# Optimization experiments

Hardware: AMD Instinct MI355X
Metric: run time of the kernel (lower is better)

Reference implementation:

```python
import jax, jax.numpy as jnp
import numpy as np

VOCAB = 50000
EDIM = 128
CDIM = 128
B = 512
LEVEL_FACTORS = [4, 4, 3, 3, 2, 1]  # 7 levels total, N = 403968 nodes


def _build_forest():
    """Deterministic random forest: per-level arrays of token, global parent idx, depth, batch id."""
    rng = np.random.default_rng(0)
    level_sizes = [B]
    for f in LEVEL_FACTORS:
        level_sizes.append(level_sizes[-1] * f)
    offsets = np.cumsum([0] + level_sizes)
    tokens = [rng.integers(0, VOCAB, B)]
    parent = [np.zeros(B, np.int64)]          # roots: dummy parent (depth 0 never scattered)
    depth = [np.zeros(B, np.int64)]
    batch_id = [np.arange(B)]
    for d in range(1, len(level_sizes)):
        n = level_sizes[d]
        tokens.append(rng.integers(0, VOCAB, n))
        p_local = rng.integers(0, level_sizes[d - 1], n)
        parent.append(offsets[d - 1] + p_local)
        depth.append(np.full(n, d, np.int64))
        batch_id.append(batch_id[d - 1][p_local])
    cat = lambda xs: np.concatenate(xs).astype(np.int32)
    return cat(tokens), cat(parent), cat(depth), cat(batch_id), len(level_sizes)


def setup_inputs() -> dict:
    key = jax.random.key(0)
    k1, k2, k3 = jax.random.split(key, 3)
    emb_table = jax.random.normal(k1, (VOCAB, EDIM), dtype=jnp.float32) * 0.02
    W = jax.random.normal(k2, (CDIM, EDIM), dtype=jnp.float32) * 0.02
    b = jax.random.normal(k3, (CDIM,), dtype=jnp.float32) * 0.02
    tokens, parent, depth, batch_id, num_levels = _build_forest()
    return {
        "emb_table": emb_table,
        "W": W,
        "b": b,
        "tokens": jnp.asarray(tokens),
        "parent": jnp.asarray(parent),
        "depth": jnp.asarray(depth),
        "batch_id": jnp.asarray(batch_id),
        "num_levels": num_levels,
        "batch_size": B,
    }


def reference(emb_table, W, b, tokens, parent, depth, batch_id, num_levels, batch_size):
    N = tokens.shape[0]
    # per-node base: W_c(embedding(token))  [N, CDIM]
    base = emb_table[tokens] @ W.T + b
    h = base
    # bottom-up subtree sum, level-batched scatter-add (deepest level first)
    for d in range(num_levels - 1, 0, -1):
        contrib = jnp.where((depth == d)[:, None], h, 0.0)
        h = h + jax.ops.segment_sum(contrib, parent, num_segments=N)
    # per-batch elementwise max over all nodes of the tree, clamped at 0
    # (original maxes zero-initialized snapshots over all recursion calls)
    out = jax.ops.segment_max(h, batch_id, num_segments=batch_size)
    return jnp.maximum(out, 0.0)
```

## Files before the change

### kernel.cpp

```cpp
#include <hip/hip_runtime.h>
#include <hip/hip_bf16.h>


using f32x4   = __attribute__((ext_vector_type(4))) float;
using short8  = __attribute__((ext_vector_type(8))) short;
using ushort8 = __attribute__((ext_vector_type(8))) unsigned short;
using float4v = __attribute__((ext_vector_type(4))) float;

#define N_ALL   403968
#define N_NONRT 403456
#define N_PAR   256512
#define OFF3    10752
#define OFF4    35328
#define OFF5    109056
#define OFF6    256512
#define SEG5    108544
#define LEAFSEG 256000
#define NVOCAB  50000
#define CAPW    384
#define D1CAP   24
#define D2CAP   64
#define WEMB_BLOCKS 782

__device__ __forceinline__ short f2bf(float f) {
  union { float f; unsigned u; } v; v.f = f;
  unsigned r = v.u + 0x7fffu + ((v.u >> 16) & 1u);
  return (short)(r >> 16);
}
__device__ __forceinline__ float bf2f(unsigned short u) {
  union { unsigned u; float f; } v; v.u = ((unsigned)u) << 16; return v.f;
}

__global__ __launch_bounds__(256) void prep_k(const float* __restrict__ W,
                                              const float* __restrict__ emb,
                                              const float* __restrict__ bias,
                                              unsigned short* __restrict__ Wemb,
                                              const int* __restrict__ parent,
                                              int* __restrict__ cnt) {
  if (blockIdx.x >= WEMB_BLOCKS) {
    int i = (blockIdx.x - WEMB_BLOCKS) * 256 + threadIdx.x + 512;
    atomicAdd(cnt + parent[i], 1);
    return;
  }
  __shared__ short WBs[16384];
  for (int idx = threadIdx.x; idx < 16384; idx += 256) {
    int j = idx & 7, c16 = (idx >> 3) & 15, g = (idx >> 7) & 3,
        s = (idx >> 9) & 3, t = idx >> 11;
    WBs[idx] = f2bf(W[(t * 16 + c16) * 128 + s * 32 + g * 8 + j]);
  }
  __syncthreads();

  const int tid = threadIdx.x, lane = tid & 63, wv = tid >> 6;
  const int l15 = lane & 15, g = lane >> 4;
  const int nb = blockIdx.x * 64 + wv * 16;

  f32x4 acc[8];
  #pragma unroll
  for (int t = 0; t < 8; ++t) {
    const float bb = bias[t * 16 + l15];
    #pragma unroll
    for (int j = 0; j < 4; ++j) acc[t][j] = bb;
  }
  int vr = nb + l15; if (vr > NVOCAB - 1) vr = NVOCAB - 1;
  const float* erow = emb + (size_t)vr * 128;
  short8 a[4];
  #pragma unroll
  for (int s = 0; s < 4; ++s) {
    float4v f0 = *(const float4v*)(erow + s * 32 + g * 8);
    float4v f1 = *(const float4v*)(erow + s * 32 + g * 8 + 4);
    short8 t;
    t[0] = f2bf(f0[0]); t[1] = f2bf(f0[1]); t[2] = f2bf(f0[2]); t[3] = f2bf(f0[3]);
    t[4] = f2bf(f1[0]); t[5] = f2bf(f1[1]); t[6] = f2bf(f1[2]); t[7] = f2bf(f1[3]);
    a[s] = t;
  }
  #pragma unroll
  for (int t = 0; t < 8; ++t) {
    #pragma unroll
    for (int s = 0; s < 4; ++s) {
      const short8 bfr = *(const short8*)&WBs[((((t * 4 + s) * 4) + g) * 16 + l15) * 8];
      acc[t] = __builtin_amdgcn_mfma_f32_16x16x32_bf16(a[s], bfr, acc[t], 0, 0, 0);
    }
  }
  #pragma unroll
  for (int j = 0; j < 4; ++j) {
    const int r = nb + g * 4 + j;
    if (r < NVOCAB) {
      ushort8 hv;
      #pragma unroll
      for (int t = 0; t < 8; ++t) hv[t] = (unsigned short)f2bf(acc[t][j]);
      *(ushort8*)(Wemb + (size_t)r * 128 + l15 * 8) = hv;
    }
  }
}

__device__ __forceinline__ int block_excl_scan(int v, int* total) {
  int lane = threadIdx.x & 63, wv = threadIdx.x >> 6;
  int x = v;
  #pragma unroll
  for (int d = 1; d < 64; d <<= 1) { int y = __shfl_up(x, d); if (lane >= d) x += y; }
  __shared__ int ws[4];
  if (lane == 63) ws[wv] = x;
  __syncthreads();
  int off = 0;
  for (int w = 0; w < wv; ++w) off += ws[w];
  __syncthreads();
  if (total) { int t = 0; for (int w = 0; w < 4; ++w) t += ws[w]; *total = t; }
  return x + off - v;
}

__global__ __launch_bounds__(256) void scanA(const int* __restrict__ cnt,
                                             int* __restrict__ start,
                                             int* __restrict__ bsum) {
  int i = blockIdx.x * 256 + threadIdx.x;
  int v = cnt[i];
  int tot;
  int ex = block_excl_scan(v, &tot);
  start[i] = ex;
  if (threadIdx.x == 0) bsum[blockIdx.x] = tot;
}

__global__ __launch_bounds__(256) void addcopy(int* __restrict__ start,
                                               int* __restrict__ start_mut,
                                               const int* __restrict__ bsum) {
  __shared__ int wsum[4];
  __shared__ int pfx;
  int partial = 0;
  for (int j = threadIdx.x; j < blockIdx.x; j += 256) partial += bsum[j];
  #pragma unroll
  for (int d = 32; d > 0; d >>= 1) partial += __shfl_down(partial, d);
  const int lane = threadIdx.x & 63, wv = threadIdx.x >> 6;
  if (lane == 0) wsum[wv] = partial;
  __syncthreads();
  if (threadIdx.x == 0) pfx = wsum[0] + wsum[1] + wsum[2] + wsum[3];
  __syncthreads();
  int i = blockIdx.x * 256 + threadIdx.x;
  int s = start[i] + pfx;
  start[i] = s; start_mut[i] = s;
  if (i == 0) start[N_PAR] = N_NONRT;
}

__global__ __launch_bounds__(256) void fill_k(const int* __restrict__ parent,
                                              const int* __restrict__ tokens,
                                              const int* __restrict__ start,
                                              int* __restrict__ start_mut,
                                              int* __restrict__ chlist,
                                              int* __restrict__ tok5s,
                                              int* __restrict__ meta5) {
  int i = blockIdx.x * 256 + threadIdx.x + 512;
  int p = atomicAdd(start_mut + parent[i], 1);
  chlist[p] = (i >= OFF6) ? tokens[i] : i;
  if (i >= OFF5 && i < OFF6) {
    const int s = p - SEG5;
    tok5s[s] = tokens[i];
    meta5[s] = ((start[i] - LEAFSEG) << 6) | (start[i + 1] - start[i]);
  }
}

__global__ __launch_bounds__(256, 8) void d4f_k(
    const unsigned short* __restrict__ Wemb,
    const int*   __restrict__ tokens,
    const int*   __restrict__ start,
    const int*   __restrict__ chlist,
    const int*   __restrict__ tok5s,
    const int*   __restrict__ meta5,
    unsigned short* __restrict__ Hout)
{
  const int chunk = threadIdx.x & 15;
  const int node  = threadIdx.x >> 4;
  const int nd    = blockIdx.x * 16 + node;
  const int gid   = OFF4 + nd;

  float acc[8], mx[8];
  {
    const int tok = tokens[gid];
    const ushort8 b = *(const ushort8*)(Wemb + (size_t)tok * 128 + chunk * 8);
    #pragma unroll
    for (int t = 0; t < 8; ++t) { acc[t] = bf2f(b[t]); mx[t] = 0.0f; }
  }

  const int s5 = start[gid] - SEG5;
  const int e5 = start[gid + 1] - SEG5;
  for (int c = s5; c < e5; ++c) {
    const int tok5 = tok5s[c];
    const int m    = meta5[c];
    const int lb   = LEAFSEG + (m >> 6);
    const int lc   = m & 63;
    const ushort8 r5 = *(const ushort8*)(Wemb + (size_t)tok5 * 128 + chunk * 8);
    float h5[8], lmx[8];
    #pragma unroll
    for (int t = 0; t < 8; ++t) { h5[t] = bf2f(r5[t]); lmx[t] = 0.0f; }
    for (int l = lb; l < lb + lc; ++l) {
      const int tl = chlist[l];
      const ushort8 rl = *(const ushort8*)(Wemb + (size_t)tl * 128 + chunk * 8);
      #pragma unroll
      for (int t = 0; t < 8; ++t) {
        const float hv = bf2f(rl[t]);
        h5[t] += hv;
        lmx[t] = fmaxf(lmx[t], hv);
      }
    }
    #pragma unroll
    for (int t = 0; t < 8; ++t) {
      acc[t] += h5[t];
      mx[t] = fmaxf(mx[t], fmaxf(lmx[t], h5[t]));
    }
  }

  ushort8 hv, mv;
  #pragma unroll
  for (int t = 0; t < 8; ++t) {
    hv[t] = (unsigned short)f2bf(acc[t]);
    mv[t] = (unsigned short)f2bf(fmaxf(mx[t], acc[t]));
  }
  __builtin_nontemporal_store(hv, (ushort8*)(Hout + (size_t)nd * 256 + chunk * 8));
  __builtin_nontemporal_store(mv, (ushort8*)(Hout + (size_t)nd * 256 + 128 + chunk * 8));
}

__global__ __launch_bounds__(256, 4) void d3_k(
    const unsigned short* __restrict__ Wemb,
    const int*   __restrict__ tokens,
    const unsigned short* __restrict__ Hin,
    unsigned short*       __restrict__ Hout,
    const int*   __restrict__ start,
    const int*   __restrict__ chlist)
{
  __shared__ int chl[CAPW];
  const int chunk = threadIdx.x & 15;
  const int node  = threadIdx.x >> 4;
  const int nd    = blockIdx.x * 16 + node;
  const int gid   = OFF3 + nd;

  int bcs = start[OFF3 + blockIdx.x * 16];
  const int bce = start[OFF3 + blockIdx.x * 16 + 16];
  const int nw  = bce - bcs;
  bool useLds = (nw <= CAPW);
  if (useLds)
    for (int i = threadIdx.x; i < nw; i += 256)
      chl[i] = chlist[bcs + i] - OFF4;
  __syncthreads();

  float acc[8], mx[8];
  {
    const int tok = tokens[gid];
    const ushort8 b = *(const ushort8*)(Wemb + (size_t)tok * 128 + chunk * 8);
    #pragma unroll
    for (int t = 0; t < 8; ++t) { acc[t] = bf2f(b[t]); mx[t] = 0.0f; }
  }

  int k = start[gid];
  const int e = start[gid + 1];
  for (; k + 2 <= e; k += 2) {
    int c0, c1;
    if (useLds) { c0 = chl[k - bcs]; c1 = chl[k + 1 - bcs]; }
    else        { c0 = chlist[k] - OFF4; c1 = chlist[k + 1] - OFF4; }
    const ushort8 h0 = *(const ushort8*)(Hin + (size_t)c0 * 256 + chunk * 8);
    const ushort8 m0 = *(const ushort8*)(Hin + (size_t)c0 * 256 + 128 + chunk * 8);
    const ushort8 h1 = *(const ushort8*)(Hin + (size_t)c1 * 256 + chunk * 8);
    const ushort8 m1 = *(const ushort8*)(Hin + (size_t)c1 * 256 + 128 + chunk * 8);
    #pragma unroll
    for (int t = 0; t < 8; ++t) {
      acc[t] += bf2f(h0[t]); mx[t] = fmaxf(mx[t], bf2f(m0[t]));
      acc[t] += bf2f(h1[t]); mx[t] = fmaxf(mx[t], bf2f(m1[t]));
    }
  }
  if (k < e) {
    int c0 = useLds ? chl[k - bcs] : chlist[k] - OFF4;
    const ushort8 h0 = *(const ushort8*)(Hin + (size_t)c0 * 256 + chunk * 8);
    const ushort8 m0 = *(const ushort8*)(Hin + (size_t)c0 * 256 + 128 + chunk * 8);
    #pragma unroll
    for (int t = 0; t < 8; ++t) {
      acc[t] += bf2f(h0[t]); mx[t] = fmaxf(mx[t], bf2f(m0[t]));
    }
  }

  ushort8 hv, mv;
  #pragma unroll
  for (int t = 0; t < 8; ++t) {
    hv[t] = (unsigned short)f2bf(acc[t]);
    mv[t] = (unsigned short)f2bf(fmaxf(mx[t], acc[t]));
  }
  *(ushort8*)(Hout + (size_t)nd * 256 + chunk * 8) = hv;
  *(ushort8*)(Hout + (size_t)nd * 256 + 128 + chunk * 8) = mv;
}

__global__ __launch_bounds__(256, 2) void top_k(
    const unsigned short* __restrict__ Wemb,
    const int*   __restrict__ tokens,
    const unsigned short* __restrict__ Hd3,
    float*       __restrict__ outf,
    const int*   __restrict__ start,
    const int*   __restrict__ chlist)
{
  __shared__ int d1id[D1CAP];
  __shared__ int c2[D1CAP];
  __shared__ int d2off[D1CAP + 1];
  __shared__ int d2id[D2CAP];
  __shared__ int n2s;
  __shared__ unsigned short rec2[D2CAP][256];
  __shared__ unsigned short rec1[D1CAP][256];

  const int r   = blockIdx.x;
  const int tid = threadIdx.x;
  const int chunk = tid & 15, grp = tid >> 4;

  const int s1 = start[r];
  int n1 = start[r + 1] - s1; if (n1 > D1CAP) n1 = D1CAP;
  if (tid < n1) {
    const int g1 = chlist[s1 + tid];
    d1id[tid] = g1;
    c2[tid] = start[g1 + 1] - start[g1];
  }
  __syncthreads();
  if (tid == 0) {
    int run = 0;
    for (int i = 0; i < n1; ++i) {
      d2off[i] = run; run += c2[i];
      if (run > D2CAP) run = D2CAP;
    }
    d2off[n1] = run; n2s = run;
  }
  __syncthreads();
  const int n2 = n2s;
  if (tid < n1) {
    const int g1 = d1id[tid];
    const int s = start[g1], o = d2off[tid], cmax = d2off[tid + 1] - o;
    for (int q = 0; q < cmax; ++q) d2id[o + q] = chlist[s + q];
  }
  __syncthreads();

  for (int i = grp; i < n2; i += 16) {
    const int g2 = d2id[i];
    float acc[8], mx[8];
    {
      const ushort8 b = *(const ushort8*)(Wemb + (size_t)tokens[g2] * 128 + chunk * 8);
      #pragma unroll
      for (int t = 0; t < 8; ++t) { acc[t] = bf2f(b[t]); mx[t] = 0.0f; }
    }
    const int e = start[g2 + 1];
    for (int k = start[g2]; k < e; ++k) {
      const int c3 = chlist[k] - OFF3;
      const ushort8 h0 = *(const ushort8*)(Hd3 + (size_t)c3 * 256 + chunk * 8);
      const ushort8 m0 = *(const ushort8*)(Hd3 + (size_t)c3 * 256 + 128 + chunk * 8);
      #pragma unroll
      for (int t = 0; t < 8; ++t) {
        acc[t] += bf2f(h0[t]); mx[t] = fmaxf(mx[t], bf2f(m0[t]));
      }
    }
    #pragma unroll
    for (int t = 0; t < 8; ++t) {
      rec2[i][chunk * 8 + t] = (unsigned short)f2bf(acc[t]);
      rec2[i][128 + chunk * 8 + t] =
          (unsigned short)f2bf(fmaxf(mx[t], acc[t]));
    }
  }
  __syncthreads();

  for (int i = grp; i < n1; i += 16) {
    const int g1 = d1id[i];
    float acc[8], mx[8];
    {
      const ushort8 b = *(const ushort8*)(Wemb + (size_t)tokens[g1] * 128 + chunk * 8);
      #pragma unroll
      for (int t = 0; t < 8; ++t) { acc[t] = bf2f(b[t]); mx[t] = 0.0f; }
    }
    for (int q = d2off[i]; q < d2off[i + 1]; ++q) {
      #pragma unroll
      for (int t = 0; t < 8; ++t) {
        acc[t] += bf2f(rec2[q][chunk * 8 + t]);
        mx[t] = fmaxf(mx[t], bf2f(rec2[q][128 + chunk * 8 + t]));
      }
    }
    #pragma unroll
    for (int t = 0; t < 8; ++t) {
      rec1[i][chunk * 8 + t] = (unsigned short)f2bf(acc[t]);
      rec1[i][128 + chunk * 8 + t] =
          (unsigned short)f2bf(fmaxf(mx[t], acc[t]));
    }
  }
  __syncthreads();

  if (grp == 0) {
    float acc[8], mx[8];
    {
      const ushort8 b = *(const ushort8*)(Wemb + (size_t)tokens[r] * 128 + chunk * 8);
      #pragma unroll
      for (int t = 0; t < 8; ++t) { acc[t] = bf2f(b[t]); mx[t] = 0.0f; }
    }
    for (int i = 0; i < n1; ++i) {
      #pragma unroll
      for (int t = 0; t < 8; ++t) {
        acc[t] += bf2f(rec1[i][chunk * 8 + t]);
        mx[t] = fmaxf(mx[t], bf2f(rec1[i][128 + chunk * 8 + t]));
      }
    }
    #pragma unroll
    for (int t = 0; t < 8; ++t)
      outf[(size_t)r * 128 + t * 16 + chunk] = fmaxf(mx[t], acc[t]);
  }
}

extern "C" void kernel_launch(void* const* d_in, const int* in_sizes, int n_in,
                              void* d_out, int out_size, void* d_ws, size_t ws_size,
                              hipStream_t stream) {
  (void)in_sizes; (void)n_in; (void)out_size; (void)ws_size;

  const float* emb    = (const float*)d_in[0];
  const float* W      = (const float*)d_in[1];
  const float* bias   = (const float*)d_in[2];
  const int*   tokens = (const int*)d_in[3];
  const int*   parent = (const int*)d_in[4];

  char* p = (char*)d_ws;
  unsigned short* bufB  = (unsigned short*)p;
  unsigned short* bufA  = (unsigned short*)(p + 75497472);
  int*   chlist   = (int*)(p + 113246208);
  int*   start    = (int*)(p + 114860032);
  int*   cnt      = (int*)(p + 115886084);
  int*   bsum     = (int*)(p + 116912132);
  unsigned short* Wemb = (unsigned short*)(p + 116949008);
  int*   tok5s    = (int*)(p + 129749008);
  int*   meta5    = (int*)(p + 130338832);

  float* outf = (float*)d_out;

  hipMemsetAsync(cnt, 0, (size_t)N_PAR * 4, stream);
  prep_k<<<WEMB_BLOCKS + N_NONRT / 256, 256, 0, stream>>>(
      W, emb, bias, Wemb, parent, cnt);
  scanA<<<N_PAR / 256, 256, 0, stream>>>(cnt, start, bsum);
  addcopy<<<N_PAR / 256, 256, 0, stream>>>(start, cnt , bsum);
  fill_k<<<N_NONRT / 256, 256, 0, stream>>>(parent, tokens, start,
                                            cnt , chlist,
                                            tok5s, meta5);

  d4f_k<<<73728 / 16, 256, 0, stream>>>(Wemb, tokens, start, chlist,
                                        tok5s, meta5, bufA);
  d3_k<<<24576 / 16, 256, 0, stream>>>(Wemb, tokens, bufA, bufB, start, chlist);
  top_k<<<512, 256, 0, stream>>>(Wemb, tokens, bufB, outf, start, chlist);
}
```

Measured before the change: 135.8 us.

## Map one wavefront per node in d4f and d3 kernels with scalar indices

Both the d4f and d3 kernels switch from 16 threads per node with 16-byte loads to one 64-lane wavefront per node, where each lane handles a 4-byte pair of bf16 values. The node index is made wave-uniform via readfirstlane, so child-list and metadata loads become scalar. The LDS staging of child indices in d3 is removed. This is meant to shorten the serial per-node loops and reduce divergence between nodes with different child counts, at the cost of narrower per-lane memory transactions and four times as many blocks.

```diff
diff --git a/kernel.cpp b/kernel.cpp
--- a/kernel.cpp
+++ b/kernel.cpp
@@ -17,7 +17,6 @@
 #define SEG5    108544
 #define LEAFSEG 256000
 #define NVOCAB  50000
-#define CAPW    384
 #define D1CAP   24
 #define D2CAP   64
 #define WEMB_BLOCKS 782
@@ -29,6 +28,12 @@
 }
 __device__ __forceinline__ float bf2f(unsigned short u) {
   union { unsigned u; float f; } v; v.u = ((unsigned)u) << 16; return v.f;
+}
+__device__ __forceinline__ float lo_bf(unsigned v) {
+  union { unsigned u; float f; } x; x.u = v << 16; return x.f;
+}
+__device__ __forceinline__ float hi_bf(unsigned v) {
+  union { unsigned u; float f; } x; x.u = v & 0xffff0000u; return x.f;
 }
 
 __global__ __launch_bounds__(256) void prep_k(const float* __restrict__ W,
@@ -165,17 +170,17 @@
     const int*   __restrict__ meta5,
     unsigned short* __restrict__ Hout)
 {
-  const int chunk = threadIdx.x & 15;
-  const int node  = threadIdx.x >> 4;
-  const int nd    = blockIdx.x * 16 + node;
-  const int gid   = OFF4 + nd;
-
-  float acc[8], mx[8];
+  const int lane = threadIdx.x & 63;
+  const int nd = __builtin_amdgcn_readfirstlane(blockIdx.x * 4 + (threadIdx.x >> 6));
+  const int gid = OFF4 + nd;
+
+  const unsigned* __restrict__ WembU = (const unsigned*)Wemb;
+
+  float acc0, acc1, mx0 = 0.0f, mx1 = 0.0f;
   {
     const int tok = tokens[gid];
-    const ushort8 b = *(const ushort8*)(Wemb + (size_t)tok * 128 + chunk * 8);
-    #pragma unroll
-    for (int t = 0; t < 8; ++t) { acc[t] = bf2f(b[t]); mx[t] = 0.0f; }
+    const unsigned bv = WembU[(size_t)tok * 64 + lane];
+    acc0 = lo_bf(bv); acc1 = hi_bf(bv);
   }
 
   const int s5 = start[gid] - SEG5;
@@ -185,38 +190,31 @@
     const int m    = meta5[c];
     const int lb   = LEAFSEG + (m >> 6);
     const int lc   = m & 63;
-    const ushort8 r5 = *(const ushort8*)(Wemb + (size_t)tok5 * 128 + chunk * 8);
-    float h5[8], lmx[8];
-    #pragma unroll
-    for (int t = 0; t < 8; ++t) { h5[t] = bf2f(r5[t]); lmx[t] = 0.0f; }
+    const unsigned r5 = WembU[(size_t)tok5 * 64 + lane];
+    float h0 = lo_bf(r5), h1 = hi_bf(r5);
+    float l0 = 0.0f, l1 = 0.0f;
     for (int l = lb; l < lb + lc; ++l) {
       const int tl = chlist[l];
-      const ushort8 rl = *(const ushort8*)(Wemb + (size_t)tl * 128 + chunk * 8);
-      #pragma unroll
-      for (int t = 0; t < 8; ++t) {
-        const float hv = bf2f(rl[t]);
-        h5[t] += hv;
-        lmx[t] = fmaxf(lmx[t], hv);
-      }
-    }
-    #pragma unroll
-    for (int t = 0; t < 8; ++t) {
-      acc[t] += h5[t];
-      mx[t] = fmaxf(mx[t], fmaxf(lmx[t], h5[t]));
-    }
-  }
-
-  ushort8 hv, mv;
-  #pragma unroll
-  for (int t = 0; t < 8; ++t) {
-    hv[t] = (unsigned short)f2bf(acc[t]);
-    mv[t] = (unsigned short)f2bf(fmaxf(mx[t], acc[t]));
-  }
-  __builtin_nontemporal_store(hv, (ushort8*)(Hout + (size_t)nd * 256 + chunk * 8));
-  __builtin_nontemporal_store(mv, (ushort8*)(Hout + (size_t)nd * 256 + 128 + chunk * 8));
-}
-
-__global__ __launch_bounds__(256, 4) void d3_k(
+      const unsigned rl = WembU[(size_t)tl * 64 + lane];
+      const float f0 = lo_bf(rl), f1 = hi_bf(rl);
+      h0 += f0; h1 += f1;
+      l0 = fmaxf(l0, f0); l1 = fmaxf(l1, f1);
+    }
+    acc0 += h0; acc1 += h1;
+    mx0 = fmaxf(mx0, fmaxf(l0, h0));
+    mx1 = fmaxf(mx1, fmaxf(l1, h1));
+  }
+
+  const unsigned ph = ((unsigned)(unsigned short)f2bf(acc1) << 16) |
+                      (unsigned)(unsigned short)f2bf(acc0);
+  const unsigned pm = ((unsigned)(unsigned short)f2bf(fmaxf(mx1, acc1)) << 16) |
+                      (unsigned)(unsigned short)f2bf(fmaxf(mx0, acc0));
+  unsigned* HoutU = (unsigned*)Hout;
+  __builtin_nontemporal_store(ph, HoutU + (size_t)nd * 128 + lane);
+  __builtin_nontemporal_store(pm, HoutU + (size_t)nd * 128 + 64 + lane);
+}
+
+__global__ __launch_bounds__(256, 8) void d3_k(
     const unsigned short* __restrict__ Wemb,
     const int*   __restrict__ tokens,
     const unsigned short* __restrict__ Hin,
@@ -224,63 +222,36 @@
     const int*   __restrict__ start,
     const int*   __restrict__ chlist)
 {
-  __shared__ int chl[CAPW];
-  const int chunk = threadIdx.x & 15;
-  const int node  = threadIdx.x >> 4;
-  const int nd    = blockIdx.x * 16 + node;
-  const int gid   = OFF3 + nd;
-
-  int bcs = start[OFF3 + blockIdx.x * 16];
-  const int bce = start[OFF3 + blockIdx.x * 16 + 16];
-  const int nw  = bce - bcs;
-  bool useLds = (nw <= CAPW);
-  if (useLds)
-    for (int i = threadIdx.x; i < nw; i += 256)
-      chl[i] = chlist[bcs + i] - OFF4;
-  __syncthreads();
-
-  float acc[8], mx[8];
+  const int lane = threadIdx.x & 63;
+  const int nd = __builtin_amdgcn_readfirstlane(blockIdx.x * 4 + (threadIdx.x >> 6));
+  const int gid = OFF3 + nd;
+
+  const unsigned* __restrict__ WembU = (const unsigned*)Wemb;
+  const unsigned* __restrict__ HinU  = (const unsigned*)Hin;
+
+  float acc0, acc1, mx0 = 0.0f, mx1 = 0.0f;
   {
     const int tok = tokens[gid];
-    const ushort8 b = *(const ushort8*)(Wemb + (size_t)tok * 128 + chunk * 8);
-    #pragma unroll
-    for (int t = 0; t < 8; ++t) { acc[t] = bf2f(b[t]); mx[t] = 0.0f; }
-  }
-
-  int k = start[gid];
+    const unsigned bv = WembU[(size_t)tok * 64 + lane];
+    acc0 = lo_bf(bv); acc1 = hi_bf(bv);
+  }
+
   const int e = start[gid + 1];
-  for (; k + 2 <= e; k += 2) {
-    int c0, c1;
-    if (useLds) { c0 = chl[k - bcs]; c1 = chl[k + 1 - bcs]; }
-    else        { c0 = chlist[k] - OFF4; c1 = chlist[k + 1] - OFF4; }
-    const ushort8 h0 = *(const ushort8*)(Hin + (size_t)c0 * 256 + chunk * 8);
-    const ushort8 m0 = *(const ushort8*)(Hin + (size_t)c0 * 256 + 128 + chunk * 8);
-    const ushort8 h1 = *(const ushort8*)(Hin + (size_t)c1 * 256 + chunk * 8);
-    const ushort8 m1 = *(const ushort8*)(Hin + (size_t)c1 * 256 + 128 + chunk * 8);
-    #pragma unroll
-    for (int t = 0; t < 8; ++t) {
-      acc[t] += bf2f(h0[t]); mx[t] = fmaxf(mx[t], bf2f(m0[t]));
-      acc[t] += bf2f(h1[t]); mx[t] = fmaxf(mx[t], bf2f(m1[t]));
-    }
-  }
-  if (k < e) {
-    int c0 = useLds ? chl[k - bcs] : chlist[k] - OFF4;
-    const ushort8 h0 = *(const ushort8*)(Hin + (size_t)c0 * 256 + chunk * 8);
-    const ushort8 m0 = *(const ushort8*)(Hin + (size_t)c0 * 256 + 128 + chunk * 8);
-    #pragma unroll
-    for (int t = 0; t < 8; ++t) {
-      acc[t] += bf2f(h0[t]); mx[t] = fmaxf(mx[t], bf2f(m0[t]));
-    }
-  }
-
-  ushort8 hv, mv;
-  #pragma unroll
-  for (int t = 0; t < 8; ++t) {
-    hv[t] = (unsigned short)f2bf(acc[t]);
-    mv[t] = (unsigned short)f2bf(fmaxf(mx[t], acc[t]));
-  }
-  *(ushort8*)(Hout + (size_t)nd * 256 + chunk * 8) = hv;
-  *(ushort8*)(Hout + (size_t)nd * 256 + 128 + chunk * 8) = mv;
+  for (int k = start[gid]; k < e; ++k) {
+    const int c = chlist[k] - OFF4;
+    const unsigned hv = HinU[(size_t)c * 128 + lane];
+    const unsigned mv = HinU[(size_t)c * 128 + 64 + lane];
+    acc0 += lo_bf(hv); acc1 += hi_bf(hv);
+    mx0 = fmaxf(mx0, lo_bf(mv)); mx1 = fmaxf(mx1, hi_bf(mv));
+  }
+
+  const unsigned ph = ((unsigned)(unsigned short)f2bf(acc1) << 16) |
+                      (unsigned)(unsigned short)f2bf(acc0);
+  const unsigned pm = ((unsigned)(unsigned short)f2bf(fmaxf(mx1, acc1)) << 16) |
+                      (unsigned)(unsigned short)f2bf(fmaxf(mx0, acc0));
+  unsigned* HoutU = (unsigned*)Hout;
+  HoutU[(size_t)nd * 128 + lane] = ph;
+  HoutU[(size_t)nd * 128 + 64 + lane] = pm;
 }
 
 __global__ __launch_bounds__(256, 2) void top_k(
@@ -432,8 +403,8 @@
                                             cnt , chlist,
                                             tok5s, meta5);
 
-  d4f_k<<<73728 / 16, 256, 0, stream>>>(Wemb, tokens, start, chlist,
-                                        tok5s, meta5, bufA);
-  d3_k<<<24576 / 16, 256, 0, stream>>>(Wemb, tokens, bufA, bufB, start, chlist);
+  d4f_k<<<73728 / 4, 256, 0, stream>>>(Wemb, tokens, start, chlist,
+                                       tok5s, meta5, bufA);
+  d3_k<<<24576 / 4, 256, 0, stream>>>(Wemb, tokens, bufA, bufB, start, chlist);
   top_k<<<512, 256, 0, stream>>>(Wemb, tokens, bufB, outf, start, chlist);
 }
```

Result: slower. 148.2 us (+9.1%).
